# Performance work log

Measured on AMD Instinct MI355X. Metric: run time of the kernel, lower is better.

The kernel has to match this reference:

```python
import jax, jax.numpy as jnp
import numpy as np

B, T, S, D, H = 16, 2048, 2048, 1024, 24  # batch, text len, encoded len, feature dim, head dim


def setup_inputs() -> dict:
    key = jax.random.key(0)
    ks = jax.random.split(key, 6)
    return {
        "encoded": jax.random.normal(ks[0], (B, S, D), dtype=jnp.float32),
        "text": jax.random.normal(ks[1], (B, T, D), dtype=jnp.float32),
        "wq": jax.random.normal(ks[2], (D, H), dtype=jnp.float32) * 0.02,
        "wk": jax.random.normal(ks[3], (D, H), dtype=jnp.float32) * 0.02,
        "wv": jax.random.normal(ks[4], (D, H), dtype=jnp.float32) * 0.02,
        "wh": jax.random.normal(ks[5], (H, D), dtype=jnp.float32) * 0.02,
    }


def reference(encoded, text, wq, wk, wv, wh):
    q = text @ wq          # [B, T, H]
    k = encoded @ wk       # [B, S, H]
    v = encoded @ wv       # [B, S, H]
    a = jnp.einsum("bth,bsh->bts", q, k)   # [B, T, S]
    # NOTE: original applies softmax over dim=1 (the QUERY axis), not the key axis.
    a = jax.nn.softmax(a, axis=1)
    h1 = jnp.einsum("bts,bsh->bth", a, v)  # [B, T, H]
    return h1 @ wh         # [B, T, D]
```

## Files before the change

### kernel.cpp

```cpp
#include <hip/hip_runtime.h>
#include <hip/hip_bf16.h>

#define B_ 16
#define T_ 2048
#define S_ 2048
#define D_ 1024
#define H_ 24
#define NROW_ (B_ * T_)
#define BS_ (B_ * S_)
#define QN32_ ((size_t)NROW_ * 32)

typedef float f32x16 __attribute__((ext_vector_type(16)));
typedef __bf16 bf16x8 __attribute__((ext_vector_type(8)));

union B8u { int4 i; bf16x8 b; };
__device__ inline bf16x8 pun(int4 v) { B8u u; u.i = v; return u.b; }

__device__ inline ushort f2bf(float f) {
  uint u = __float_as_uint(f);
  u += 0x7fffu + ((u >> 16) & 1u);
  return (ushort)(u >> 16);
}
__device__ inline float bf2f(ushort u) { return __uint_as_float(((uint)u) << 16); }

__device__ inline f32x16 mfma32(bf16x8 a, bf16x8 b, f32x16 c) {
  return __builtin_amdgcn_mfma_f32_32x32x16_bf16(a, b, c, 0, 0, 0);
}

__device__ inline uint cvtpk(float a, float b) {
  uint r;
  asm("v_cvt_pk_bf16_f32 %0, %1, %2" : "=v"(r) : "v"(a), "v"(b));
  return r;
}

__global__ __launch_bounds__(256) void prep_w(
    const float* __restrict__ wq, const float* __restrict__ wk,
    const float* __restrict__ wv, ushort* __restrict__ wpk) {
  int i = blockIdx.x * 256 + threadIdx.x;
  if (i >= 3 * 128 * H_) return;
  int which = i / (128 * H_);
  int rem = i - which * 128 * H_;
  int k8g = rem / H_, n = rem - k8g * H_;
  const float* w = (which == 0) ? wq : (which == 1) ? wk : wv;
  ushort t[8];
#pragma unroll
  for (int j = 0; j < 8; ++j) t[j] = f2bf(w[(k8g * 8 + j) * H_ + n]);
  *(int4*)&wpk[(size_t)i * 8] = *(const int4*)t;
}


#define LOADG(dst, g)                                                        \
  _Pragma("unroll") for (int j = 0; j < 8; ++j) dst[j] =                     \
      *(const float4*)(rowp + (size_t)((g) * 8 + j) * D_ + l * 4);
#define WRITEG(src, g)                                                       \
  _Pragma("unroll") for (int j = 0; j < 8; ++j) {                            \
    const int row = (g) * 8 + j;                                             \
    uint p0 = cvtpk(src[j].x, src[j].y), p1 = cvtpk(src[j].z, src[j].w);     \
    const int s = (l >> 1) ^ (row & 7);                                      \
    *(uint2*)&sA[w][row][s * 8 + (l & 1) * 4] = make_uint2(p0, p1);          \
  }

__global__ __launch_bounds__(256, 2) void proj_q(
    const float* __restrict__ in, const ushort* __restrict__ wpk,
    ushort* __restrict__ qb) {
  __shared__ __align__(16) ushort sA[4][32][256];

  const int tid = threadIdx.x;
  const int lane = tid & 63, lo = lane & 31, hi = lane >> 5, w = tid >> 6;
  const int l = lane;
  const long rowbase = (long)blockIdx.x * 32;
  const int ne = (lo < H_) ? lo : 0;
  const float* rowp = in + rowbase * D_ + w * 256;

  float4 ga[8], gb[8];
  LOADG(ga, 0); LOADG(gb, 1);
  WRITEG(ga, 0); LOADG(ga, 2);
  WRITEG(gb, 1); LOADG(gb, 3);
  WRITEG(ga, 2); WRITEG(gb, 3);

  int4 bfr[16];
#pragma unroll
  for (int c = 0; c < 16; ++c) {
    const int k8g = w * 32 + 2 * c + hi;
    bfr[c] = *(const int4*)&wpk[(size_t)(k8g * H_ + ne) * 8];
  }
  f32x16 acc = {};
#pragma unroll
  for (int c = 0; c < 16; ++c) {
    const int s = (2 * c + hi) ^ (lo & 7);
    bf16x8 a = pun(*(const int4*)&sA[w][lo][s * 8]);
    acc = mfma32(a, pun(bfr[c]), acc);
  }

  float* sR = (float*)sA;
  __syncthreads();
#pragma unroll
  for (int r = 0; r < 16; ++r) sR[w * 1088 + lane * 17 + r] = acc[r];
  __syncthreads();
  const int qd = tid >> 6, l2 = tid & 63, lo2 = l2 & 31, hi2 = l2 >> 5;
#pragma unroll
  for (int rr = 0; rr < 4; ++rr) {
    const int r = qd * 4 + rr;
    float s = sR[0 * 1088 + l2 * 17 + r] + sR[1 * 1088 + l2 * 17 + r] +
              sR[2 * 1088 + l2 * 17 + r] + sR[3 * 1088 + l2 * 17 + r];
    const int mrow = rr + 8 * qd + 4 * hi2;
    qb[(size_t)(rowbase + mrow) * 32 + lo2] = (lo2 < H_) ? f2bf(s) : (ushort)0;
  }
}

__global__ __launch_bounds__(256, 2) void proj_kv(
    const float* __restrict__ in, const ushort* __restrict__ wpk,
    ushort* __restrict__ kbuf, float* __restrict__ vv) {
  __shared__ __align__(16) ushort sA[4][32][256];

  const int tid = threadIdx.x;
  const int lane = tid & 63, lo = lane & 31, hi = lane >> 5, w = tid >> 6;
  const int l = lane;
  const long rowbase = (long)blockIdx.x * 32;
  const int ne = (lo < H_) ? lo : 0;
  const float* rowp = in + rowbase * D_ + w * 256;
  const ushort* wp1 = wpk + (size_t)1 * 128 * H_ * 8;
  const ushort* wp2 = wpk + (size_t)2 * 128 * H_ * 8;

  float4 ga[8], gb[8];
  LOADG(ga, 0); LOADG(gb, 1);
  WRITEG(ga, 0); LOADG(ga, 2);
  WRITEG(gb, 1); LOADG(gb, 3);
  WRITEG(ga, 2); WRITEG(gb, 3);

  int4 bfr1[16], bfr2[16];
#pragma unroll
  for (int c = 0; c < 16; ++c) {
    const int k8g = w * 32 + 2 * c + hi;
    bfr1[c] = *(const int4*)&wp1[(size_t)(k8g * H_ + ne) * 8];
    bfr2[c] = *(const int4*)&wp2[(size_t)(k8g * H_ + ne) * 8];
  }
  f32x16 acc = {};
  f32x16 acc2 = {};
#pragma unroll
  for (int c = 0; c < 16; ++c) {
    const int s = (2 * c + hi) ^ (lo & 7);
    bf16x8 a = pun(*(const int4*)&sA[w][lo][s * 8]);
    acc = mfma32(a, pun(bfr1[c]), acc);
    acc2 = mfma32(a, pun(bfr2[c]), acc2);
  }

  float* sR = (float*)sA;
  __syncthreads();
#pragma unroll
  for (int r = 0; r < 16; ++r) sR[w * 1088 + lane * 17 + r] = acc[r];
  __syncthreads();
  {
    const int qd = tid >> 6, l2 = tid & 63, lo2 = l2 & 31, hi2 = l2 >> 5;
#pragma unroll
    for (int rr = 0; rr < 4; ++rr) {
      const int r = qd * 4 + rr;
      float s = sR[0 * 1088 + l2 * 17 + r] + sR[1 * 1088 + l2 * 17 + r] +
                sR[2 * 1088 + l2 * 17 + r] + sR[3 * 1088 + l2 * 17 + r];
      const int mrow = rr + 8 * qd + 4 * hi2;
      kbuf[(size_t)(rowbase + mrow) * 32 + lo2] =
          (lo2 < H_) ? f2bf(s) : (ushort)0;
    }
  }
  __syncthreads();
#pragma unroll
  for (int r = 0; r < 16; ++r) sR[w * 1088 + lane * 17 + r] = acc2[r];
  __syncthreads();
  {
    const int qd = tid >> 6, l2 = tid & 63, lo2 = l2 & 31, hi2 = l2 >> 5;
    if (lo2 < H_) {
#pragma unroll
      for (int rr = 0; rr < 4; ++rr) {
        const int r = qd * 4 + rr;
        float s = sR[0 * 1088 + l2 * 17 + r] + sR[1 * 1088 + l2 * 17 + r] +
                  sR[2 * 1088 + l2 * 17 + r] + sR[3 * 1088 + l2 * 17 + r];
        const int mrow = rr + 8 * qd + 4 * hi2;
        vv[(size_t)(rowbase + mrow) * H_ + lo2] = s;
      }
    }
  }
}
#undef LOADG
#undef WRITEG

__global__ __launch_bounds__(256) void colsum_mfma(
    const ushort* __restrict__ qb, const ushort* __restrict__ kb,
    float* __restrict__ dpart) {
  __shared__ __align__(16) ushort sQ[4 * 32 * 8];
  const int tid = threadIdx.x;
  const int lane = tid & 63;
  const int lo = lane & 31, hi = lane >> 5;
  const int w = tid >> 6;
  const int b = blockIdx.y;
  const int s0 = blockIdx.x * 128 + w * 32;
  const int tpart = blockIdx.z;

  const ushort* krow = kb + ((size_t)b * S_ + s0 + lo) * 32;
  bf16x8 k0 = pun(*(const int4*)(krow + hi * 8));
  bf16x8 k1 = pun(*(const int4*)(krow + 16 + hi * 8));

  float dl = 0.f;
  for (int tc = 0; tc < 16; ++tc) {
    const int tbase = tpart * 512 + tc * 32;
    if (tid < 128) {
      int t = tid >> 2, j = tid & 3;
      *(int4*)&sQ[j * 256 + t * 8] =
          *(const int4*)(qb + ((size_t)b * T_ + tbase + t) * 32 + j * 8);
    }
    __syncthreads();
    bf16x8 qa = pun(*(const int4*)&sQ[hi * 256 + lo * 8]);
    bf16x8 qc = pun(*(const int4*)&sQ[(2 + hi) * 256 + lo * 8]);
    f32x16 c = {};
    c = mfma32(qa, k0, c);
    c = mfma32(qc, k1, c);
#pragma unroll
    for (int r = 0; r < 16; ++r) dl += __expf(c[r]);
    __syncthreads();
  }
  dl += __shfl_xor(dl, 32);
  if (hi == 0) dpart[(size_t)tpart * BS_ + (size_t)b * S_ + s0 + lo] = dl;
}

__global__ __launch_bounds__(256) void vscale_kernel(
    const float* __restrict__ vv, const float* __restrict__ dpart,
    ushort* __restrict__ vsT) {
  int gid = blockIdx.x * 256 + threadIdx.x;
  int s4 = gid & 511;
  int h = (gid >> 9) & 31;
  int b = gid >> 14;
  int s0 = s4 * 4;
  ushort4 ov;
  if (h < H_) {
    const float* vp = vv + ((size_t)b * S_ + s0) * H_ + h;
    const float* dp = dpart + (size_t)b * S_ + s0;
    float dv[4];
#pragma unroll
    for (int i = 0; i < 4; ++i) {
      float d = dp[i] + dp[BS_ + i] + dp[2 * BS_ + i] + dp[3 * BS_ + i];
      dv[i] = 1.0f / d;
    }
    ov.x = f2bf(vp[0 * H_] * dv[0]);
    ov.y = f2bf(vp[1 * H_] * dv[1]);
    ov.z = f2bf(vp[2 * H_] * dv[2]);
    ov.w = f2bf(vp[3 * H_] * dv[3]);
  } else {
    ov.x = ov.y = ov.z = ov.w = 0;
  }
  *(ushort4*)&vsT[((size_t)b * 32 + h) * S_ + s0] = ov;
}

__global__ __launch_bounds__(256) void attn_mfma(
    const ushort* __restrict__ qb, const ushort* __restrict__ kb,
    const ushort* __restrict__ vsT, ushort* __restrict__ h1p) {
  __shared__ __align__(16) ushort sK[4 * 32 * 8];
  __shared__ __align__(16) ushort sV[4 * 32 * 8];
  const int tid = threadIdx.x;
  const int lane = tid & 63;
  const int lo = lane & 31, hi = lane >> 5;
  const int w = tid >> 6;
  const int b = blockIdx.y;
  const int t0 = blockIdx.x * 128 + w * 32;
  const int spart = blockIdx.z;

  const ushort* qrow = qb + ((size_t)b * T_ + t0 + lo) * 32;
  bf16x8 q0 = pun(*(const int4*)(qrow + hi * 8));
  bf16x8 q1 = pun(*(const int4*)(qrow + 16 + hi * 8));

  f32x16 hacc = {};
  for (int sc = 0; sc < 16; ++sc) {
    const int sbase = spart * 512 + sc * 32;
    if (tid < 128) {
      int s = tid >> 2, j = tid & 3;
      *(int4*)&sK[j * 256 + s * 8] =
          *(const int4*)(kb + ((size_t)b * S_ + sbase + s) * 32 + j * 8);
    } else {
      int i2 = tid - 128;
      int h = i2 >> 2, q = i2 & 3;
      *(int4*)&sV[q * 256 + h * 8] =
          *(const int4*)(vsT + ((size_t)b * 32 + h) * S_ + sbase + q * 8);
    }
    __syncthreads();
    bf16x8 ka = pun(*(const int4*)&sK[hi * 256 + lo * 8]);
    bf16x8 kc = pun(*(const int4*)&sK[(2 + hi) * 256 + lo * 8]);
    bf16x8 va = pun(*(const int4*)&sV[hi * 256 + lo * 8]);
    bf16x8 vc = pun(*(const int4*)&sV[(2 + hi) * 256 + lo * 8]);
    f32x16 c = {};
    c = mfma32(ka, q0, c);
    c = mfma32(kc, q1, c);
    uint pk[8];
#pragma unroll
    for (int m = 0; m < 8; ++m) {
      float plo = __expf(c[2 * m]);
      float phi = __expf(c[2 * m + 1]);
      pk[m] = cvtpk(plo, phi);
    }
    asm("v_permlane32_swap_b32 %0, %1" : "+v"(pk[0]), "+v"(pk[2]));
    asm("v_permlane32_swap_b32 %0, %1" : "+v"(pk[1]), "+v"(pk[3]));
    asm("v_permlane32_swap_b32 %0, %1" : "+v"(pk[4]), "+v"(pk[6]));
    asm("v_permlane32_swap_b32 %0, %1" : "+v"(pk[5]), "+v"(pk[7]));
    int4 f0 = make_int4(pk[0], pk[1], pk[2], pk[3]);
    int4 f1 = make_int4(pk[4], pk[5], pk[6], pk[7]);
    hacc = mfma32(pun(f0), va, hacc);
    hacc = mfma32(pun(f1), vc, hacc);
    __syncthreads();
  }
  ushort* o = h1p + (size_t)spart * QN32_ + (size_t)b * T_ * 32;
#pragma unroll
  for (int r = 0; r < 16; ++r) {
    int trow = t0 + (r & 3) + 8 * (r >> 2) + 4 * hi;
    o[(size_t)trow * 32 + lo] = f2bf(hacc[r]);
  }
}

__global__ __launch_bounds__(256) void out_kernel(const ushort* __restrict__ h1p,
                                                  const float* __restrict__ wh,
                                                  float* __restrict__ out) {
  __shared__ __align__(16) float s_h1[16 * 24];
  const int tid = threadIdx.x;
  const long rbase = (long)blockIdx.x * 16;
  if (tid < 48) {
    const int r = tid / 3, c8 = tid - 3 * r;
    float s[8] = {0.f, 0.f, 0.f, 0.f, 0.f, 0.f, 0.f, 0.f};
#pragma unroll
    for (int part = 0; part < 4; ++part) {
      int4 v = *(const int4*)&h1p[(size_t)part * QN32_ +
                                  (size_t)(rbase + r) * 32 + c8 * 8];
      const ushort* u = (const ushort*)&v;
#pragma unroll
      for (int j = 0; j < 8; ++j) s[j] += bf2f(u[j]);
    }
#pragma unroll
    for (int j = 0; j < 8; ++j) s_h1[r * 24 + c8 * 8 + j] = s[j];
  }
  __syncthreads();
  for (int c = 0; c < 4; ++c) {
    const int dd = c * 256 + tid;
    float wr[24];
#pragma unroll
    for (int h = 0; h < 24; ++h) wr[h] = wh[h * D_ + dd];
#pragma unroll 1
    for (int r = 0; r < 16; ++r) {
      float a = 0.f;
#pragma unroll
      for (int j = 0; j < 6; ++j) {
        float4 hv = *(const float4*)(s_h1 + r * 24 + 4 * j);
        a = fmaf(hv.x, wr[4 * j], a);
        a = fmaf(hv.y, wr[4 * j + 1], a);
        a = fmaf(hv.z, wr[4 * j + 2], a);
        a = fmaf(hv.w, wr[4 * j + 3], a);
      }
      out[(rbase + r) * D_ + dd] = a;
    }
  }
}

extern "C" void kernel_launch(void* const* d_in, const int* in_sizes, int n_in,
                              void* d_out, int out_size, void* d_ws,
                              size_t ws_size, hipStream_t stream) {
  const float* encoded = (const float*)d_in[0];
  const float* text = (const float*)d_in[1];
  const float* wq = (const float*)d_in[2];
  const float* wk = (const float*)d_in[3];
  const float* wv = (const float*)d_in[4];
  const float* wh = (const float*)d_in[5];
  float* out = (float*)d_out;

  ushort* qb = (ushort*)d_ws;
  ushort* kbuf = qb + QN32_;
  float* vv = (float*)(kbuf + QN32_);
  float* dpart = vv + (size_t)BS_ * H_;
  ushort* vsT = (ushort*)(dpart + 4 * BS_);
  ushort* h1p = vsT + (size_t)B_ * 32 * S_;
  ushort* wpk = h1p + 4 * QN32_;

  prep_w<<<36, 256, 0, stream>>>(wq, wk, wv, wpk);
  proj_q<<<1024, 256, 0, stream>>>(text, wpk, qb);
  proj_kv<<<1024, 256, 0, stream>>>(encoded, wpk, kbuf, vv);
  colsum_mfma<<<dim3(S_ / 128, B_, 4), 256, 0, stream>>>(qb, kbuf, dpart);
  vscale_kernel<<<(B_ * 32 * (S_ / 4)) / 256, 256, 0, stream>>>(vv, dpart, vsT);
  attn_mfma<<<dim3(T_ / 128, B_, 4), 256, 0, stream>>>(qb, kbuf, vsT, h1p);
  out_kernel<<<NROW_ / 16, 256, 0, stream>>>(h1p, wh, out);
}
```

Baseline: 164.2 us.

## Double per-wave tile in colsum and attention, swizzle proj blocks, nontemporal output

```diff
diff --git a/kernel.cpp b/kernel.cpp
--- a/kernel.cpp
+++ b/kernel.cpp
@@ -48,7 +48,6 @@
   *(int4*)&wpk[(size_t)i * 8] = *(const int4*)t;
 }
 
-
 #define LOADG(dst, g)                                                        \
   _Pragma("unroll") for (int j = 0; j < 8; ++j) dst[j] =                     \
       *(const float4*)(rowp + (size_t)((g) * 8 + j) * D_ + l * 4);
@@ -68,7 +67,8 @@
   const int tid = threadIdx.x;
   const int lane = tid & 63, lo = lane & 31, hi = lane >> 5, w = tid >> 6;
   const int l = lane;
-  const long rowbase = (long)blockIdx.x * 32;
+  const int bid = (blockIdx.x & 7) * 128 + (blockIdx.x >> 3);
+  const long rowbase = (long)bid * 32;
   const int ne = (lo < H_) ? lo : 0;
   const float* rowp = in + rowbase * D_ + w * 256;
 
@@ -116,7 +116,8 @@
   const int tid = threadIdx.x;
   const int lane = tid & 63, lo = lane & 31, hi = lane >> 5, w = tid >> 6;
   const int l = lane;
-  const long rowbase = (long)blockIdx.x * 32;
+  const int bid = (blockIdx.x & 7) * 128 + (blockIdx.x >> 3);
+  const long rowbase = (long)bid * 32;
   const int ne = (lo < H_) ? lo : 0;
   const float* rowp = in + rowbase * D_ + w * 256;
   const ushort* wp1 = wpk + (size_t)1 * 128 * H_ * 8;
@@ -192,14 +193,18 @@
   const int lo = lane & 31, hi = lane >> 5;
   const int w = tid >> 6;
   const int b = blockIdx.y;
-  const int s0 = blockIdx.x * 128 + w * 32;
+  const int s0 = blockIdx.x * 256 + w * 32;
+  const int s1 = s0 + 128;
   const int tpart = blockIdx.z;
 
-  const ushort* krow = kb + ((size_t)b * S_ + s0 + lo) * 32;
-  bf16x8 k0 = pun(*(const int4*)(krow + hi * 8));
-  bf16x8 k1 = pun(*(const int4*)(krow + 16 + hi * 8));
-
-  float dl = 0.f;
+  const ushort* krow0 = kb + ((size_t)b * S_ + s0 + lo) * 32;
+  bf16x8 k0 = pun(*(const int4*)(krow0 + hi * 8));
+  bf16x8 k1 = pun(*(const int4*)(krow0 + 16 + hi * 8));
+  const ushort* krow1 = kb + ((size_t)b * S_ + s1 + lo) * 32;
+  bf16x8 k2 = pun(*(const int4*)(krow1 + hi * 8));
+  bf16x8 k3 = pun(*(const int4*)(krow1 + 16 + hi * 8));
+
+  float dl = 0.f, dl2 = 0.f;
   for (int tc = 0; tc < 16; ++tc) {
     const int tbase = tpart * 512 + tc * 32;
     if (tid < 128) {
@@ -215,10 +220,19 @@
     c = mfma32(qc, k1, c);
 #pragma unroll
     for (int r = 0; r < 16; ++r) dl += __expf(c[r]);
+    f32x16 c2 = {};
+    c2 = mfma32(qa, k2, c2);
+    c2 = mfma32(qc, k3, c2);
+#pragma unroll
+    for (int r = 0; r < 16; ++r) dl2 += __expf(c2[r]);
     __syncthreads();
   }
   dl += __shfl_xor(dl, 32);
-  if (hi == 0) dpart[(size_t)tpart * BS_ + (size_t)b * S_ + s0 + lo] = dl;
+  dl2 += __shfl_xor(dl2, 32);
+  if (hi == 0) {
+    dpart[(size_t)tpart * BS_ + (size_t)b * S_ + s0 + lo] = dl;
+    dpart[(size_t)tpart * BS_ + (size_t)b * S_ + s1 + lo] = dl2;
+  }
 }
 
 __global__ __launch_bounds__(256) void vscale_kernel(
@@ -259,14 +273,19 @@
   const int lo = lane & 31, hi = lane >> 5;
   const int w = tid >> 6;
   const int b = blockIdx.y;
-  const int t0 = blockIdx.x * 128 + w * 32;
+  const int t0 = blockIdx.x * 256 + w * 32;
+  const int t1 = t0 + 128;
   const int spart = blockIdx.z;
 
-  const ushort* qrow = qb + ((size_t)b * T_ + t0 + lo) * 32;
-  bf16x8 q0 = pun(*(const int4*)(qrow + hi * 8));
-  bf16x8 q1 = pun(*(const int4*)(qrow + 16 + hi * 8));
+  const ushort* qrow0 = qb + ((size_t)b * T_ + t0 + lo) * 32;
+  bf16x8 q0 = pun(*(const int4*)(qrow0 + hi * 8));
+  bf16x8 q1 = pun(*(const int4*)(qrow0 + 16 + hi * 8));
+  const ushort* qrow1 = qb + ((size_t)b * T_ + t1 + lo) * 32;
+  bf16x8 q2 = pun(*(const int4*)(qrow1 + hi * 8));
+  bf16x8 q3 = pun(*(const int4*)(qrow1 + 16 + hi * 8));
 
   f32x16 hacc = {};
+  f32x16 hacc2 = {};
   for (int sc = 0; sc < 16; ++sc) {
     const int sbase = spart * 512 + sc * 32;
     if (tid < 128) {
@@ -284,31 +303,54 @@
     bf16x8 kc = pun(*(const int4*)&sK[(2 + hi) * 256 + lo * 8]);
     bf16x8 va = pun(*(const int4*)&sV[hi * 256 + lo * 8]);
     bf16x8 vc = pun(*(const int4*)&sV[(2 + hi) * 256 + lo * 8]);
-    f32x16 c = {};
-    c = mfma32(ka, q0, c);
-    c = mfma32(kc, q1, c);
-    uint pk[8];
-#pragma unroll
-    for (int m = 0; m < 8; ++m) {
-      float plo = __expf(c[2 * m]);
-      float phi = __expf(c[2 * m + 1]);
-      pk[m] = cvtpk(plo, phi);
-    }
-    asm("v_permlane32_swap_b32 %0, %1" : "+v"(pk[0]), "+v"(pk[2]));
-    asm("v_permlane32_swap_b32 %0, %1" : "+v"(pk[1]), "+v"(pk[3]));
-    asm("v_permlane32_swap_b32 %0, %1" : "+v"(pk[4]), "+v"(pk[6]));
-    asm("v_permlane32_swap_b32 %0, %1" : "+v"(pk[5]), "+v"(pk[7]));
-    int4 f0 = make_int4(pk[0], pk[1], pk[2], pk[3]);
-    int4 f1 = make_int4(pk[4], pk[5], pk[6], pk[7]);
-    hacc = mfma32(pun(f0), va, hacc);
-    hacc = mfma32(pun(f1), vc, hacc);
+    {
+      f32x16 c = {};
+      c = mfma32(ka, q0, c);
+      c = mfma32(kc, q1, c);
+      uint pk[8];
+#pragma unroll
+      for (int m = 0; m < 8; ++m) {
+        float plo = __expf(c[2 * m]);
+        float phi = __expf(c[2 * m + 1]);
+        pk[m] = cvtpk(plo, phi);
+      }
+      asm("v_permlane32_swap_b32 %0, %1" : "+v"(pk[0]), "+v"(pk[2]));
+      asm("v_permlane32_swap_b32 %0, %1" : "+v"(pk[1]), "+v"(pk[3]));
+      asm("v_permlane32_swap_b32 %0, %1" : "+v"(pk[4]), "+v"(pk[6]));
+      asm("v_permlane32_swap_b32 %0, %1" : "+v"(pk[5]), "+v"(pk[7]));
+      int4 f0 = make_int4(pk[0], pk[1], pk[2], pk[3]);
+      int4 f1 = make_int4(pk[4], pk[5], pk[6], pk[7]);
+      hacc = mfma32(pun(f0), va, hacc);
+      hacc = mfma32(pun(f1), vc, hacc);
+    }
+    {
+      f32x16 c = {};
+      c = mfma32(ka, q2, c);
+      c = mfma32(kc, q3, c);
+      uint pk[8];
+#pragma unroll
+      for (int m = 0; m < 8; ++m) {
+        float plo = __expf(c[2 * m]);
+        float phi = __expf(c[2 * m + 1]);
+        pk[m] = cvtpk(plo, phi);
+      }
+      asm("v_permlane32_swap_b32 %0, %1" : "+v"(pk[0]), "+v"(pk[2]));
+      asm("v_permlane32_swap_b32 %0, %1" : "+v"(pk[1]), "+v"(pk[3]));
+      asm("v_permlane32_swap_b32 %0, %1" : "+v"(pk[4]), "+v"(pk[6]));
+      asm("v_permlane32_swap_b32 %0, %1" : "+v"(pk[5]), "+v"(pk[7]));
+      int4 f0 = make_int4(pk[0], pk[1], pk[2], pk[3]);
+      int4 f1 = make_int4(pk[4], pk[5], pk[6], pk[7]);
+      hacc2 = mfma32(pun(f0), va, hacc2);
+      hacc2 = mfma32(pun(f1), vc, hacc2);
+    }
     __syncthreads();
   }
   ushort* o = h1p + (size_t)spart * QN32_ + (size_t)b * T_ * 32;
 #pragma unroll
   for (int r = 0; r < 16; ++r) {
-    int trow = t0 + (r & 3) + 8 * (r >> 2) + 4 * hi;
-    o[(size_t)trow * 32 + lo] = f2bf(hacc[r]);
+    int rr = (r & 3) + 8 * (r >> 2) + 4 * hi;
+    o[(size_t)(t0 + rr) * 32 + lo] = f2bf(hacc[r]);
+    o[(size_t)(t1 + rr) * 32 + lo] = f2bf(hacc2[r]);
   }
 }
 
@@ -349,7 +391,7 @@
         a = fmaf(hv.z, wr[4 * j + 2], a);
         a = fmaf(hv.w, wr[4 * j + 3], a);
       }
-      out[(rbase + r) * D_ + dd] = a;
+      __builtin_nontemporal_store(a, &out[(rbase + r) * D_ + dd]);
     }
   }
 }
@@ -376,8 +418,8 @@
   prep_w<<<36, 256, 0, stream>>>(wq, wk, wv, wpk);
   proj_q<<<1024, 256, 0, stream>>>(text, wpk, qb);
   proj_kv<<<1024, 256, 0, stream>>>(encoded, wpk, kbuf, vv);
-  colsum_mfma<<<dim3(S_ / 128, B_, 4), 256, 0, stream>>>(qb, kbuf, dpart);
+  colsum_mfma<<<dim3(S_ / 256, B_, 4), 256, 0, stream>>>(qb, kbuf, dpart);
   vscale_kernel<<<(B_ * 32 * (S_ / 4)) / 256, 256, 0, stream>>>(vv, dpart, vsT);
-  attn_mfma<<<dim3(T_ / 128, B_, 4), 256, 0, stream>>>(qb, kbuf, vsT, h1p);
+  attn_mfma<<<dim3(T_ / 256, B_, 4), 256, 0, stream>>>(qb, kbuf, vsT, h1p);
   out_kernel<<<NROW_ / 16, 256, 0, stream>>>(h1p, wh, out);
 }
```

Measured after the change: 138.4 us. 15.7% less time.
